# Kernel optimization log

Measured on AMD Instinct MI355X. Metric: run time of the kernel, lower is better.

Reference implementation:

```python
import jax, jax.numpy as jnp
import numpy as np

BS, N, D = 8, 2048, 512


def setup_inputs() -> dict:
    key = jax.random.key(0)
    ks = jax.random.split(key, 8)
    s = 0.05  # small scale keeps exp(k + bias) numerically tame
    inp = jax.random.normal(ks[0], (BS, N, D), dtype=jnp.float32)
    Wq = jax.random.normal(ks[1], (D, D), dtype=jnp.float32) * s
    bq = jax.random.normal(ks[2], (D,), dtype=jnp.float32) * s
    Wk = jax.random.normal(ks[3], (D, D), dtype=jnp.float32) * s
    bk = jax.random.normal(ks[4], (D,), dtype=jnp.float32) * s
    Wv = jax.random.normal(ks[5], (D, D), dtype=jnp.float32) * s
    bv = jax.random.normal(ks[6], (D,), dtype=jnp.float32) * s
    pos_bias = jax.random.normal(ks[7], (N, N), dtype=jnp.float32) * s
    return {"input": inp, "Wq": Wq, "bq": bq, "Wk": Wk, "bk": bk,
            "Wv": Wv, "bv": bv, "pos_bias": pos_bias}


def reference(input, Wq, bq, Wk, bk, Wv, bv, pos_bias):
    # q, k, v projections: (bs, n, d)
    q = input @ Wq + bq
    k = input @ Wk + bk
    v = input @ Wv + bv
    # AFT-Full: out[b,i,d] = sigmoid(q)[b,i,d] *
    #   sum_j exp(k[b,j,d] + B[i,j]) * v[b,j,d] / sum_j exp(k[b,j,d] + B[i,j])
    # Factor exp(k + B) = exp(B) * exp(k): avoids the (n,bs,n,d) broadcast,
    # identical math to the torch source.
    ek = jnp.exp(k)                       # (bs, n, d)
    eB = jnp.exp(pos_bias)                # (n, n), rows = query pos i
    numerator = jnp.einsum('ij,bjd->bid', eB, ek * v)
    denominator = jnp.einsum('ij,bjd->bid', eB, ek)
    return jax.nn.sigmoid(q) * (numerator / denominator)
```

## Files before the change

kernel.cpp:

```cpp
#include <hip/hip_runtime.h>
#include <stdint.h>

#define N_SEQ 2048
#define D_MODEL 512
#define MROWS 16384
#define NT_K 32

typedef __attribute__((ext_vector_type(8))) short bf16x8;
typedef __attribute__((ext_vector_type(4))) float f32x4;

__device__ __forceinline__ short f2bf(float f) {
  union { float f; uint32_t u; } x; x.f = f;
  uint32_t r = x.u + 0x7FFFu + ((x.u >> 16) & 1u);
  return (short)(uint16_t)(r >> 16);
}
__device__ __forceinline__ unsigned short f2h(float f) {
  union { _Float16 h; unsigned short u; } x; x.h = (_Float16)f; return x.u;
}
__device__ __forceinline__ float h2f(unsigned short u) {
  union { unsigned short u; _Float16 h; } x; x.u = u; return (float)x.h;
}

__device__ __forceinline__ void gload_lds16(const void* g, void* l) {
  __builtin_amdgcn_global_load_lds(
      (__attribute__((address_space(1))) void*)(void*)g,
      (__attribute__((address_space(3))) void*)l, 16, 0, 0);
}


__global__ void k_conv_bf16(const float* __restrict__ in,
                            short* __restrict__ a, int n4) {
  int stride = gridDim.x * blockDim.x;
  for (int i = blockIdx.x * blockDim.x + threadIdx.x; i < n4; i += stride) {
    float4 v = reinterpret_cast<const float4*>(in)[i];
    short4 h;
    h.x = f2bf(v.x); h.y = f2bf(v.y); h.z = f2bf(v.z); h.w = f2bf(v.w);
    reinterpret_cast<short4*>(a)[i] = h;
  }
}

__global__ void k_prep_eb(const float* __restrict__ pb, short* __restrict__ eb,
                          int n4) {
  int stride = gridDim.x * blockDim.x;
  for (int i = blockIdx.x * blockDim.x + threadIdx.x; i < n4; i += stride) {
    float4 v = reinterpret_cast<const float4*>(pb)[i];
    short4 o;
    o.x = f2bf(expf(v.x));
    o.y = f2bf(expf(v.y));
    o.z = f2bf(expf(v.z));
    o.w = f2bf(expf(v.w));
    reinterpret_cast<short4*>(eb)[i] = o;
  }
}

__global__ void k_prep_w(const float* __restrict__ Wq, const float* __restrict__ Wk,
                         const float* __restrict__ Wv, short* __restrict__ wh) {
  int t = blockIdx.x * blockDim.x + threadIdx.x;
  if (t >= 1536 * 512) return;
  int c = t >> 9, k = t & 511;
  float v;
  if (c < 512) v = Wq[k * 512 + c];
  else {
    int cc = c - 512, d = cc >> 1;
    v = (cc & 1) ? Wv[k * 512 + d] : Wk[k * 512 + d];
  }
  wh[t] = f2bf(v);
}

__global__ __launch_bounds__(256) void k_proj(
    const short* __restrict__ A, const short* __restrict__ W,
    const float* __restrict__ bq, const float* __restrict__ bk,
    const float* __restrict__ bv,
    unsigned short* __restrict__ sigq, short* __restrict__ Xt) {
  __shared__ short lA[128 * 64], lB[128 * 64];
  const int tid = threadIdx.x;
  const int lane = tid & 63, wid = tid >> 6;
  const int wr = wid >> 1, wc = wid & 1;
  const int lrow = lane & 15;
  const int kq = (lane >> 4) << 4;
  const int row0 = blockIdx.x * 128;
  const int col0 = blockIdx.y * 128;

  const f32x4 fzero = {0.f, 0.f, 0.f, 0.f};
  f32x4 acc[4][4];
#pragma unroll
  for (int m = 0; m < 4; ++m)
#pragma unroll
    for (int n = 0; n < 4; ++n) acc[m][n] = fzero;

  const short* gA = A + row0 * 512;
  const short* gB = W + col0 * 512;

  for (int kt = 0; kt < 8; ++kt) {
    const int kb = kt * 64;
#pragma unroll
    for (int p = 0; p < 4; ++p) {
      int c = p * 256 + tid;
      int B = c << 4;
      int r = B >> 7;
      int wp = (B & 127) ^ ((r & 7) << 4);
      int ke = wp >> 1;
      int goff = r * 512 + kb + ke;
      int loff = (p * 256 + wid * 64) << 3;
      gload_lds16(gA + goff, lA + loff);
      gload_lds16(gB + goff, lB + loff);
    }
    __syncthreads();
#pragma unroll
    for (int ks = 0; ks < 2; ++ks) {
      int kb2 = kq + ks * 64;
      bf16x8 fb[4];
#pragma unroll
      for (int n = 0; n < 4; ++n) {
        int r = wc * 64 + n * 16 + lrow;
        fb[n] = *(const bf16x8*)((const char*)lB + (r << 7) +
                                 (kb2 ^ ((r & 7) << 4)));
      }
#pragma unroll
      for (int m = 0; m < 4; ++m) {
        int r = wr * 64 + m * 16 + lrow;
        bf16x8 fa = *(const bf16x8*)((const char*)lA + (r << 7) +
                                     (kb2 ^ ((r & 7) << 4)));
#pragma unroll
        for (int n = 0; n < 4; ++n)
          acc[m][n] = __builtin_amdgcn_mfma_f32_16x16x32_bf16(fa, fb[n], acc[m][n], 0, 0, 0);
      }
    }
    __syncthreads();
  }

  const int rbase = row0 + wr * 64 + ((lane >> 4) << 2);
  if (col0 < 512) {
#pragma unroll
    for (int n = 0; n < 4; ++n) {
      int c = col0 + wc * 64 + n * 16 + lrow;
      float bias = bq[c];
#pragma unroll
      for (int m = 0; m < 4; ++m) {
        int gr = rbase + m * 16;
#pragma unroll
        for (int r = 0; r < 4; ++r) {
          float q = acc[m][n][r] + bias;
          sigq[(gr + r) * 512 + c] = f2h(1.f / (1.f + expf(-q)));
        }
      }
    }
  } else {
    int s = lane & 1;
#pragma unroll
    for (int n = 0; n < 4; ++n) {
      int c = col0 + wc * 64 + n * 16 + lrow;
      int d = (c - 512) >> 1;
      float bias = s ? bv[d] : bk[d];
#pragma unroll
      for (int m = 0; m < 4; ++m) {
        int gr = rbase + m * 16;
        int b = gr >> 11;
        int j = gr & 2047;
        f32x4 val;
#pragma unroll
        for (int r = 0; r < 4; ++r) val[r] = acc[m][n][r] + bias;
        if (!s) {
#pragma unroll
          for (int r = 0; r < 4; ++r) val[r] = expf(val[r]);
        }
        f32x4 oth;
#pragma unroll
        for (int r = 0; r < 4; ++r) oth[r] = __shfl_xor(val[r], 1);
        if (!s) {
          short4 wq, eq;
          wq.x = f2bf(val[0] * oth[0]); eq.x = f2bf(val[0]);
          wq.y = f2bf(val[1] * oth[1]); eq.y = f2bf(val[1]);
          wq.z = f2bf(val[2] * oth[2]); eq.z = f2bf(val[2]);
          wq.w = f2bf(val[3] * oth[3]); eq.w = f2bf(val[3]);
          int colp = b * 1024 + 2 * d;
          *(short4*)&Xt[colp * 2048 + j] = wq;
          *(short4*)&Xt[(colp + 1) * 2048 + j] = eq;
        }
      }
    }
  }
}


#define MM(FA, FB, NH)                                                      \
  {                                                                         \
    _Pragma("unroll") for (int mm_ = 0; mm_ < 8; ++mm_) {                   \
      acc[mm_][2 * (NH)] = __builtin_amdgcn_mfma_f32_16x16x32_bf16(         \
          FA[mm_], FB[2 * (NH)], acc[mm_][2 * (NH)], 0, 0, 0);              \
      acc[mm_][2 * (NH) + 1] = __builtin_amdgcn_mfma_f32_16x16x32_bf16(     \
          FA[mm_], FB[2 * (NH) + 1], acc[mm_][2 * (NH) + 1], 0, 0, 0);      \
    }                                                                       \
  }

#define PHASE_MID()                                     \
  __builtin_amdgcn_sched_barrier(0);                    \
  __builtin_amdgcn_s_barrier();                         \
  asm volatile("s_waitcnt lgkmcnt(0)" ::: "memory");    \
  __builtin_amdgcn_sched_barrier(0);                    \
  __builtin_amdgcn_s_setprio(1)

#define PHASE_END()                                     \
  __builtin_amdgcn_s_setprio(0);                        \
  __builtin_amdgcn_sched_barrier(0);                    \
  __builtin_amdgcn_s_barrier()

#define VMCNT4() asm volatile("s_waitcnt vmcnt(4)" ::: "memory")

__global__ __launch_bounds__(512, 1) void k_main8(
    const short* __restrict__ eB, const short* __restrict__ Xt,
    const unsigned short* __restrict__ sigq, float* __restrict__ out) {
  extern __shared__ short lds[];
  const int tid = threadIdx.x;
  const int lane = tid & 63, wid = tid >> 6;
  const int wr = wid >> 2, wc = wid & 3;
  const int lrow = lane & 15;
  const int khi = (lane >> 4) << 4;

  const int bid = blockIdx.x;
  const int xcd = bid & 7, j = bid >> 3;
  const int row0 = (j & 7) * 256;
  const int col0 = ((xcd << 2) + (j >> 3)) * 256;

  const f32x4 fzero = {0.f, 0.f, 0.f, 0.f};
  f32x4 acc[8][4];
#pragma unroll
  for (int m = 0; m < 8; ++m)
#pragma unroll
    for (int n = 0; n < 4; ++n) acc[m][n] = fzero;

  const short* gA = eB + row0 * 2048;
  const short* gB = Xt + col0 * 2048;

  auto STAGE = [&](int kt, int isB, int h) {
    int ktc = kt < NT_K ? kt : NT_K - 1;
    const short* src = (isB ? gB : gA) + (h * 128) * 2048 + ktc * 64;
    int sbase = ((ktc & 1) << 15) + (isB << 14) + (h << 13);
#pragma unroll
    for (int p = 0; p < 2; ++p) {
      int c = p * 512 + tid;
      int r = c >> 3;
      int ke = ((((c & 7) << 4) ^ ((r & 7) << 4)) >> 1);
      gload_lds16(src + r * 2048 + ke,
                  lds + sbase + ((p * 512 + wid * 64) << 3));
    }
  };
  auto LDA = [&](int buf, int ks, int m) -> bf16x8 {
    int R = wr * 128 + m * 16 + lrow;
    int kb = ks * 64 + khi;
    return *(const bf16x8*)((const char*)lds + (buf << 16) + R * 128 +
                            (kb ^ ((R & 7) << 4)));
  };
  auto LDB = [&](int buf, int ks, int n) -> bf16x8 {
    int Rc = wc * 64 + n * 16 + lrow;
    int kb = ks * 64 + khi;
    return *(const bf16x8*)((const char*)lds + (buf << 16) + 32768 +
                            Rc * 128 + (kb ^ ((Rc & 7) << 4)));
  };

  STAGE(0, 0, 0); STAGE(0, 0, 1); STAGE(0, 1, 0); STAGE(0, 1, 1);
  STAGE(1, 0, 0); STAGE(1, 0, 1);
  VMCNT4();
  __builtin_amdgcn_sched_barrier(0);
  __builtin_amdgcn_s_barrier();

  bf16x8 fa0[8], fa1[8], fb0[4], fb1[4];

  for (int it = 0; it < NT_K / 2; ++it) {
    const int t0 = 2 * it, t1 = 2 * it + 1;
#pragma unroll
    for (int m = 0; m < 8; ++m) fa0[m] = LDA(0, 0, m);
#pragma unroll
    for (int n = 0; n < 4; ++n) fb0[n] = LDB(0, 0, n);
    STAGE(t1, 1, 0);
    PHASE_MID();
    MM(fa0, fb0, 0);
    PHASE_END();
#pragma unroll
    for (int m = 0; m < 8; ++m) fa1[m] = LDA(0, 1, m);
#pragma unroll
    for (int n = 0; n < 4; ++n) fb1[n] = LDB(0, 1, n);
    STAGE(t1, 1, 1);
    PHASE_MID();
    MM(fa0, fb0, 1);
    PHASE_END();
    STAGE(t0 + 2, 0, 0);
    PHASE_MID();
    MM(fa1, fb1, 0);
    PHASE_END();
    STAGE(t0 + 2, 0, 1);
    VMCNT4();
    PHASE_MID();
    MM(fa1, fb1, 1);
    PHASE_END();
#pragma unroll
    for (int m = 0; m < 8; ++m) fa0[m] = LDA(1, 0, m);
#pragma unroll
    for (int n = 0; n < 4; ++n) fb0[n] = LDB(1, 0, n);
    STAGE(t0 + 2, 1, 0);
    PHASE_MID();
    MM(fa0, fb0, 0);
    PHASE_END();
#pragma unroll
    for (int m = 0; m < 8; ++m) fa1[m] = LDA(1, 1, m);
#pragma unroll
    for (int n = 0; n < 4; ++n) fb1[n] = LDB(1, 1, n);
    STAGE(t0 + 2, 1, 1);
    PHASE_MID();
    MM(fa0, fb0, 1);
    PHASE_END();
    STAGE(t1 + 2, 0, 0);
    PHASE_MID();
    MM(fa1, fb1, 0);
    PHASE_END();
    STAGE(t1 + 2, 0, 1);
    VMCNT4();
    PHASE_MID();
    MM(fa1, fb1, 1);
    PHASE_END();
  }

  const int rbase = row0 + wr * 128 + ((lane >> 4) << 2);
#pragma unroll
  for (int n = 0; n < 4; ++n) {
    int c = col0 + wc * 64 + n * 16 + lrow;
    int b = c >> 10;
    int d = (c & 1023) >> 1;
#pragma unroll
    for (int m = 0; m < 8; ++m) {
      f32x4 den;
#pragma unroll
      for (int r = 0; r < 4; ++r) den[r] = __shfl_xor(acc[m][n][r], 1);
      if ((lane & 1) == 0) {
#pragma unroll
        for (int r = 0; r < 4; ++r) {
          int i2 = rbase + m * 16 + r;
          int idx = (b * 2048 + i2) * 512 + d;
          out[idx] = h2f(sigq[idx]) * (acc[m][n][r] / den[r]);
        }
      }
    }
  }
}

extern "C" void kernel_launch(void* const* d_in, const int* in_sizes, int n_in,
                              void* d_out, int out_size, void* d_ws, size_t ws_size,
                              hipStream_t stream) {
  const float* in = (const float*)d_in[0];
  const float* Wq = (const float*)d_in[1];
  const float* bq = (const float*)d_in[2];
  const float* Wk = (const float*)d_in[3];
  const float* bk = (const float*)d_in[4];
  const float* Wv = (const float*)d_in[5];
  const float* bv = (const float*)d_in[6];
  const float* pb = (const float*)d_in[7];
  float* out = (float*)d_out;

  char* ws = (char*)d_ws;
  short* Xt = (short*)ws;
  short* eB = (short*)(ws + 33554432);
  short* Ah = (short*)(ws + 41943040);
  short* Wh = (short*)(ws + 58720256);
  unsigned short* sigq = (unsigned short*)(ws + 60293120);

  (void)hipFuncSetAttribute((const void*)k_main8,
                            hipFuncAttributeMaxDynamicSharedMemorySize, 131072);

  k_conv_bf16<<<2048, 256, 0, stream>>>(in, Ah, MROWS * D_MODEL / 4);
  k_prep_w<<<3072, 256, 0, stream>>>(Wq, Wk, Wv, Wh);
  k_prep_eb<<<2048, 256, 0, stream>>>(pb, eB, N_SEQ * N_SEQ / 4);

  dim3 gp(128, 12);
  k_proj<<<gp, 256, 0, stream>>>(Ah, Wh, bq, bk, bv, sigq, Xt);

  k_main8<<<dim3(256), 512, 131072, stream>>>(eB, Xt, sigq, out);
}
```

Before: 147.9 us.

## Replace eight-phase interleaved GEMM schedule with simple two-buffer per-tile pipeline

```diff
diff --git a/kernel.cpp b/kernel.cpp
--- a/kernel.cpp
+++ b/kernel.cpp
@@ -193,21 +193,7 @@
     }                                                                       \
   }
 
-#define PHASE_MID()                                     \
-  __builtin_amdgcn_sched_barrier(0);                    \
-  __builtin_amdgcn_s_barrier();                         \
-  asm volatile("s_waitcnt lgkmcnt(0)" ::: "memory");    \
-  __builtin_amdgcn_sched_barrier(0);                    \
-  __builtin_amdgcn_s_setprio(1)
-
-#define PHASE_END()                                     \
-  __builtin_amdgcn_s_setprio(0);                        \
-  __builtin_amdgcn_sched_barrier(0);                    \
-  __builtin_amdgcn_s_barrier()
-
-#define VMCNT4() asm volatile("s_waitcnt vmcnt(4)" ::: "memory")
-
-__global__ __launch_bounds__(512, 1) void k_main8(
+__global__ __launch_bounds__(512, 1) void k_main2(
     const short* __restrict__ eB, const short* __restrict__ Xt,
     const unsigned short* __restrict__ sigq, float* __restrict__ out) {
   extern __shared__ short lds[];
@@ -233,9 +219,8 @@
   const short* gB = Xt + col0 * 2048;
 
   auto STAGE = [&](int kt, int isB, int h) {
-    int ktc = kt < NT_K ? kt : NT_K - 1;
-    const short* src = (isB ? gB : gA) + (h * 128) * 2048 + ktc * 64;
-    int sbase = ((ktc & 1) << 15) + (isB << 14) + (h << 13);
+    const short* src = (isB ? gB : gA) + (h * 128) * 2048 + kt * 64;
+    int sbase = ((kt & 1) << 15) + (isB << 14) + (h << 13);
 #pragma unroll
     for (int p = 0; p < 2; ++p) {
       int c = p * 512 + tid;
@@ -259,65 +244,37 @@
   };
 
   STAGE(0, 0, 0); STAGE(0, 0, 1); STAGE(0, 1, 0); STAGE(0, 1, 1);
-  STAGE(1, 0, 0); STAGE(1, 0, 1);
-  VMCNT4();
-  __builtin_amdgcn_sched_barrier(0);
-  __builtin_amdgcn_s_barrier();
-
-  bf16x8 fa0[8], fa1[8], fb0[4], fb1[4];
-
-  for (int it = 0; it < NT_K / 2; ++it) {
-    const int t0 = 2 * it, t1 = 2 * it + 1;
-#pragma unroll
-    for (int m = 0; m < 8; ++m) fa0[m] = LDA(0, 0, m);
-#pragma unroll
-    for (int n = 0; n < 4; ++n) fb0[n] = LDB(0, 0, n);
-    STAGE(t1, 1, 0);
-    PHASE_MID();
+  STAGE(1, 0, 0); STAGE(1, 0, 1); STAGE(1, 1, 0); STAGE(1, 1, 1);
+
+  for (int t = 0; t < NT_K; ++t) {
+    const int b = t & 1;
+    asm volatile("s_waitcnt vmcnt(8)" ::: "memory");
+    __builtin_amdgcn_sched_barrier(0);
+    __builtin_amdgcn_s_barrier();
+
+    bf16x8 fa0[8], fb0[4], fa1[8], fb1[4];
+#pragma unroll
+    for (int m = 0; m < 8; ++m) fa0[m] = LDA(b, 0, m);
+#pragma unroll
+    for (int n = 0; n < 4; ++n) fb0[n] = LDB(b, 0, n);
+    __builtin_amdgcn_s_setprio(1);
     MM(fa0, fb0, 0);
-    PHASE_END();
-#pragma unroll
-    for (int m = 0; m < 8; ++m) fa1[m] = LDA(0, 1, m);
-#pragma unroll
-    for (int n = 0; n < 4; ++n) fb1[n] = LDB(0, 1, n);
-    STAGE(t1, 1, 1);
-    PHASE_MID();
     MM(fa0, fb0, 1);
-    PHASE_END();
-    STAGE(t0 + 2, 0, 0);
-    PHASE_MID();
+    __builtin_amdgcn_s_setprio(0);
+#pragma unroll
+    for (int m = 0; m < 8; ++m) fa1[m] = LDA(b, 1, m);
+#pragma unroll
+    for (int n = 0; n < 4; ++n) fb1[n] = LDB(b, 1, n);
+    __builtin_amdgcn_s_setprio(1);
     MM(fa1, fb1, 0);
-    PHASE_END();
-    STAGE(t0 + 2, 0, 1);
-    VMCNT4();
-    PHASE_MID();
     MM(fa1, fb1, 1);
-    PHASE_END();
-#pragma unroll
-    for (int m = 0; m < 8; ++m) fa0[m] = LDA(1, 0, m);
-#pragma unroll
-    for (int n = 0; n < 4; ++n) fb0[n] = LDB(1, 0, n);
-    STAGE(t0 + 2, 1, 0);
-    PHASE_MID();
-    MM(fa0, fb0, 0);
-    PHASE_END();
-#pragma unroll
-    for (int m = 0; m < 8; ++m) fa1[m] = LDA(1, 1, m);
-#pragma unroll
-    for (int n = 0; n < 4; ++n) fb1[n] = LDB(1, 1, n);
-    STAGE(t0 + 2, 1, 1);
-    PHASE_MID();
-    MM(fa0, fb0, 1);
-    PHASE_END();
-    STAGE(t1 + 2, 0, 0);
-    PHASE_MID();
-    MM(fa1, fb1, 0);
-    PHASE_END();
-    STAGE(t1 + 2, 0, 1);
-    VMCNT4();
-    PHASE_MID();
-    MM(fa1, fb1, 1);
-    PHASE_END();
+    __builtin_amdgcn_s_setprio(0);
+
+    __builtin_amdgcn_sched_barrier(0);
+    __builtin_amdgcn_s_barrier();
+    __builtin_amdgcn_sched_barrier(0);
+    int tn = t + 2 < NT_K ? t + 2 : NT_K - 1;
+    STAGE(tn, 0, 0); STAGE(tn, 0, 1); STAGE(tn, 1, 0); STAGE(tn, 1, 1);
   }
 
   const int rbase = row0 + wr * 128 + ((lane >> 4) << 2);
@@ -363,7 +320,7 @@
   short* Wh = (short*)(ws + 58720256);
   unsigned short* sigq = (unsigned short*)(ws + 60293120);
 
-  (void)hipFuncSetAttribute((const void*)k_main8,
+  (void)hipFuncSetAttribute((const void*)k_main2,
                             hipFuncAttributeMaxDynamicSharedMemorySize, 131072);
 
   k_conv_bf16<<<2048, 256, 0, stream>>>(in, Ah, MROWS * D_MODEL / 4);
@@ -373,5 +330,5 @@
   dim3 gp(128, 12);
   k_proj<<<gp, 256, 0, stream>>>(Ah, Wh, bq, bk, bv, sigq, Xt);
 
-  k_main8<<<dim3(256), 512, 131072, stream>>>(eB, Xt, sigq, out);
-}
+  k_main2<<<dim3(256), 512, 131072, stream>>>(eB, Xt, sigq, out);
+}
```

After: 150.4 us. Within noise of the previous version (+1.7%).
